# Optimization experiments

Hardware: AMD Instinct MI355X
Metric: run time of the kernel (lower is better)

## Reference

```python
import jax, jax.numpy as jnp
import numpy as np

N, E, IN_DIM, D, T, L, B, SLEN, C = 50000, 600000, 128, 128, 4, 2, 2048, 16, 16


def _deg_inv_sqrt(idx, n, dtype):
    deg = jax.ops.segment_sum(jnp.ones(idx.shape, dtype=dtype), idx, num_segments=n)
    return jnp.where(deg > 0, deg ** -0.5, 0.0).astype(dtype)


def gcn_conv(h, edge_index, W, b):
    # PyG GCNConv: add self loops, symmetric norm, x@W, scatter-add, +bias
    n = h.shape[0]
    loop = jnp.arange(n)
    row = jnp.concatenate([edge_index[0], loop])
    col = jnp.concatenate([edge_index[1], loop])
    dis = _deg_inv_sqrt(col, n, h.dtype)
    norm = dis[row] * dis[col]              # [E+N]
    xw = h @ W                               # [N, D]
    msgs = xw[row] * norm[:, None]           # [E+N, D] gather
    out = jax.ops.segment_sum(msgs, col, num_segments=n)
    return out + b


def re_conv(r, edge_index, node_type, W, wtype, b):
    # REConv(norm='both'): left-norm by src out-degree, x@W, type weight,
    # scatter-add to dst, right-norm by dst in-degree, +bias, relu
    n = r.shape[0]
    row, col = edge_index
    dl = _deg_inv_sqrt(row, n, r.dtype)
    x = (r * dl[:, None]) @ W                # [N, T]
    x = x * wtype[node_type][:, None]
    out = jax.ops.segment_sum(x[row], col, num_segments=n)
    dr = _deg_inv_sqrt(col, n, r.dtype)
    out = out * dr[:, None] + b
    return jax.nn.relu(out)


def setup_inputs() -> dict:
    key = jax.random.key(0)
    ks = jax.random.split(key, 10)
    x = jax.random.normal(ks[0], (N, IN_DIM), dtype=jnp.float32)
    label = jax.random.randint(ks[1], (N,), 0, C)
    seqs = jax.random.randint(ks[2], (B, SLEN), 0, N)
    edge_index = jax.random.randint(ks[3], (2, E), 0, N)
    node_type = jnp.sort(jax.random.randint(ks[4], (N,), 0, T))
    s_in = 1.0 / np.sqrt(IN_DIM)
    s_d = 1.0 / np.sqrt(D)
    fcW = jax.random.normal(ks[5], (T, IN_DIM, D), dtype=jnp.float32) * s_in
    fcB = jnp.zeros((T, D), dtype=jnp.float32)
    gcnW = jax.random.normal(ks[6], (L, D, D), dtype=jnp.float32) * s_d
    gcnB = jnp.zeros((L, D), dtype=jnp.float32)
    reW = jax.random.normal(ks[7], (L, T, T), dtype=jnp.float32) * 0.5
    re_wtype = jnp.ones((L, T), dtype=jnp.float32)
    reB = jnp.zeros((L, T), dtype=jnp.float32)
    predW = jax.random.normal(ks[8], (D, C), dtype=jnp.float32) * s_d
    predB = jnp.zeros((C,), dtype=jnp.float32)
    return {"x": x, "label": label, "seqs": seqs, "edge_index": edge_index,
            "node_type": node_type, "fcW": fcW, "fcB": fcB, "gcnW": gcnW,
            "gcnB": gcnB, "reW": reW, "re_wtype": re_wtype, "reB": reB,
            "predW": predW, "predB": predB}


def reference(x, label, seqs, edge_index, node_type, fcW, fcB, gcnW, gcnB,
              reW, re_wtype, reB, predW, predB):
    n = x.shape[0]
    # per-type input projection; node_type is sorted so this equals
    # torch.cat([fc[t](x[node_type==t]) for t])
    h_all = jnp.einsum('ni,tio->tno', x, fcW) + fcB[:, None, :]  # [T, N, D]
    gh = h_all[node_type, jnp.arange(n)]                          # [N, D]
    r = jnp.eye(fcW.shape[0], dtype=x.dtype)[node_type]           # [N, T]
    for l in range(gcnW.shape[0]):
        gh = jax.nn.relu(gcn_conv(gh, edge_index, gcnW[l], gcnB[l]))
        r = re_conv(r, edge_index, node_type, reW[l], re_wtype[l], reB[l])
    ego = seqs[:, 0]
    output = gh[ego] @ predW + predB                               # [B, C]
    return output, label[ego]
```

## Files before the change

kernel.cpp:

```cpp
#include <hip/hip_runtime.h>
#include <hip/hip_bf16.h>


typedef __attribute__((ext_vector_type(8))) short short8;
typedef __attribute__((ext_vector_type(4))) float f32x4;
typedef unsigned short u16;

__device__ __forceinline__ float bf2f(u16 u) {
  union { float f; unsigned int i; } v; v.i = (unsigned int)u << 16; return v.f;
}
__device__ __forceinline__ u16 f2bf(float f) {
  union { float f; unsigned int i; } v; v.f = f;
  return (u16)((v.i + 0x7FFF + ((v.i >> 16) & 1)) >> 16);
}

#define NPB 128
#define SWZ(row, byte) ((byte) ^ (((row) & 15) << 4))

__global__ void k_prep(const float* __restrict__ fcW, const float* __restrict__ gcnW,
                       u16* __restrict__ wt, int* __restrict__ ecnt,
                       int T, int wt_total, int n) {
  const int gt = blockIdx.x * 256 + threadIdx.x;
  const int GT = gridDim.x * 256;
  for (int i = gt; i < wt_total; i += GT) {
    int m = i >> 14, dk = i & 16383, d = dk >> 7, k = dk & 127;
    const float* src = (m < T) ? (fcW + ((size_t)m << 14)) : (gcnW + ((size_t)(m - T) << 14));
    wt[i] = f2bf(src[k * 128 + d]);
  }
  for (int i = gt; i < n; i += GT) ecnt[i] = 0;
}

__device__ __forceinline__ void stage_tile_bf16(char* smem, const u16* __restrict__ gsrc,
                                                int rows_valid, int t) {
  int row = t >> 1;
  int h = (t & 1) * 64;
  int byte0 = row * 256 + h * 2;
  if (row < rows_valid) {
    const u16* src = gsrc + (size_t)row * 128 + h;
#pragma unroll
    for (int j = 0; j < 8; ++j) {
      short8 v = *(const short8*)(src + j * 8);
      *(short8*)(smem + SWZ(row, byte0 + j * 16)) = v;
    }
  } else {
    short8 z = (short8){0, 0, 0, 0, 0, 0, 0, 0};
#pragma unroll
    for (int j = 0; j < 8; ++j)
      *(short8*)(smem + SWZ(row, byte0 + j * 16)) = z;
  }
}

__device__ __forceinline__ void mfma_core128(const char* xs, const char* wt, int t,
                                             f32x4 acc[8][2]) {
  const int lane = t & 63, w = t >> 6;
  const int lr = lane & 15, lk = lane >> 4;
  short8 bfrag[4][2];
#pragma unroll
  for (int ks = 0; ks < 4; ++ks) {
    int kb = ks * 64 + lk * 16;
#pragma unroll
    for (int ch = 0; ch < 2; ++ch) {
      int row = w * 32 + ch * 16 + lr;
      bfrag[ks][ch] = *(const short8*)(wt + SWZ(row, row * 256 + kb));
    }
  }
#pragma unroll
  for (int ks = 0; ks < 4; ++ks) {
    int kb = ks * 64 + lk * 16;
    short8 a[8];
#pragma unroll
    for (int rg = 0; rg < 8; ++rg) {
      int row = rg * 16 + lr;
      a[rg] = *(const short8*)(xs + SWZ(row, row * 256 + kb));
    }
#pragma unroll
    for (int rg = 0; rg < 8; ++rg)
#pragma unroll
      for (int ch = 0; ch < 2; ++ch)
        acc[rg][ch] = __builtin_amdgcn_mfma_f32_16x16x32_bf16(a[rg], bfrag[ks][ch],
                                                              acc[rg][ch], 0, 0, 0);
  }
}

__global__ __launch_bounds__(256) void k_fc(const float* __restrict__ x,
                                            const int* __restrict__ node_type,
                                            const u16* __restrict__ wt_fc,
                                            const float* __restrict__ fcB,
                                            u16* __restrict__ gh, int n_nodes,
                                            const int* __restrict__ col,
                                            int* __restrict__ ecnt, int e_edges) {
  __shared__ char smem[65536];
  char* smem_xs = smem;
  char* smem_wt = smem + 32768;
  const int t = threadIdx.x;
  const int nbase = blockIdx.x * NPB;
  const int nend = min(nbase + NPB, n_nodes);
  const int t0 = node_type[nbase];
  const int t1 = node_type[nend - 1];

  {
    int row = t >> 1;
    int h = (t & 1) * 64;
    int node = nbase + row;
    int byte0 = row * 256 + h * 2;
    if (node < n_nodes) {
      const float4* src = (const float4*)(x + (size_t)node * 128 + h);
#pragma unroll
      for (int j = 0; j < 8; ++j) {
        float4 a4 = src[j * 2], b4 = src[j * 2 + 1];
        u16 tmp[8] = {f2bf(a4.x), f2bf(a4.y), f2bf(a4.z), f2bf(a4.w),
                      f2bf(b4.x), f2bf(b4.y), f2bf(b4.z), f2bf(b4.w)};
        *(short8*)(smem_xs + SWZ(row, byte0 + j * 16)) = *(short8*)tmp;
      }
    } else {
      short8 z = (short8){0, 0, 0, 0, 0, 0, 0, 0};
#pragma unroll
      for (int j = 0; j < 8; ++j)
        *(short8*)(smem_xs + SWZ(row, byte0 + j * 16)) = z;
    }
  }

  const int lane = t & 63, w = t >> 6;
  const int lr = lane & 15, lk = lane >> 4;

  for (int tt = t0; tt <= t1; ++tt) {
    if (tt > t0) __syncthreads();
    stage_tile_bf16(smem_wt, wt_fc + ((size_t)tt << 14), 128, t);
    __syncthreads();

    f32x4 acc[8][2];
#pragma unroll
    for (int rg = 0; rg < 8; ++rg)
#pragma unroll
      for (int ch = 0; ch < 2; ++ch) acc[rg][ch] = (f32x4){0.f, 0.f, 0.f, 0.f};
    mfma_core128(smem_xs, smem_wt, t, acc);

    float bv0 = fcB[tt * 128 + w * 32 + lr];
    float bv1 = fcB[tt * 128 + w * 32 + 16 + lr];
#pragma unroll
    for (int rg = 0; rg < 8; ++rg) {
#pragma unroll
      for (int reg = 0; reg < 4; ++reg) {
        int node = nbase + rg * 16 + lk * 4 + reg;
        if (node < n_nodes && node_type[node] == tt) {
          gh[(size_t)node * 128 + w * 32 + lr]      = f2bf(acc[rg][0][reg] + bv0);
          gh[(size_t)node * 128 + w * 32 + 16 + lr] = f2bf(acc[rg][1][reg] + bv1);
        }
      }
    }
  }

  const int gt = blockIdx.x * 256 + t;
  const int GT = gridDim.x * 256;
  for (int i = gt; i < e_edges; i += GT) atomicAdd(&ecnt[col[i]], 1);
}

__global__ __launch_bounds__(256) void k_gemm_scale(const u16* __restrict__ ghin,
                                                    const u16* __restrict__ wtg,
                                                    const float* __restrict__ dis,
                                                    u16* __restrict__ xws, int n_nodes,
                                                    const int* __restrict__ row,
                                                    const int* __restrict__ col,
                                                    int* __restrict__ cursor,
                                                    int* __restrict__ edge_row,
                                                    int e_edges, int do_fill) {
  __shared__ char smem[65536];
  char* smem_xs = smem;
  char* smem_wt = smem + 32768;
  const int t = threadIdx.x;
  const int nbase = blockIdx.x * NPB;

  stage_tile_bf16(smem_xs, ghin + (size_t)nbase * 128, min(n_nodes - nbase, NPB), t);
  stage_tile_bf16(smem_wt, wtg, 128, t);
  __syncthreads();

  f32x4 acc[8][2];
#pragma unroll
  for (int rg = 0; rg < 8; ++rg)
#pragma unroll
    for (int ch = 0; ch < 2; ++ch) acc[rg][ch] = (f32x4){0.f, 0.f, 0.f, 0.f};
  mfma_core128(smem_xs, smem_wt, t, acc);

  const int lane = t & 63, w = t >> 6;
  const int lr = lane & 15, lk = lane >> 4;
#pragma unroll
  for (int rg = 0; rg < 8; ++rg) {
#pragma unroll
    for (int reg = 0; reg < 4; ++reg) {
      int node = nbase + rg * 16 + lk * 4 + reg;
      if (node < n_nodes) {
        float s = dis[node];
        xws[(size_t)node * 128 + w * 32 + lr]      = f2bf(acc[rg][0][reg] * s);
        xws[(size_t)node * 128 + w * 32 + 16 + lr] = f2bf(acc[rg][1][reg] * s);
      }
    }
  }

  if (do_fill) {
    const int gt = blockIdx.x * 256 + t;
    const int GT = gridDim.x * 256;
    for (int i = gt; i < e_edges; i += GT) {
      int c = col[i];
      int pos = atomicAdd(&cursor[c], 1);
      edge_row[pos] = row[i];
    }
  }
}

__global__ __launch_bounds__(256) void k_scan1(const int* __restrict__ ecnt,
                                               int* __restrict__ scanex,
                                               int* __restrict__ partials, int n) {
  __shared__ int s[256];
  const int t = threadIdx.x;
  const int i = blockIdx.x * 256 + t;
  int v = (i < n) ? ecnt[i] : 0;
  s[t] = v;
  __syncthreads();
  for (int off = 1; off < 256; off <<= 1) {
    int add = (t >= off) ? s[t - off] : 0;
    __syncthreads();
    s[t] += add;
    __syncthreads();
  }
  if (i < n) scanex[i] = s[t] - v;
  if (t == 255) partials[blockIdx.x] = s[t];
}

__global__ __launch_bounds__(256) void k_scan2(int* __restrict__ partials, int np) {
  __shared__ int s[256];
  const int t = threadIdx.x;
  int v = (t < np) ? partials[t] : 0;
  s[t] = v;
  __syncthreads();
  for (int off = 1; off < 256; off <<= 1) {
    int add = (t >= off) ? s[t - off] : 0;
    __syncthreads();
    s[t] += add;
    __syncthreads();
  }
  if (t < np) partials[t] = s[t] - v;
}

__global__ void k_scan3(const int* __restrict__ scanex, const int* __restrict__ partials,
                        const int* __restrict__ ecnt, int* __restrict__ col_ptr,
                        int* __restrict__ cursor, float* __restrict__ dis,
                        int n, int e_total) {
  int i = blockIdx.x * 256 + threadIdx.x;
  if (i < n) {
    int p = scanex[i] + partials[i >> 8];
    col_ptr[i] = p;
    cursor[i] = p;
    dis[i] = rsqrtf((float)(ecnt[i] + 1));
  }
  if (i == 0) col_ptr[n] = e_total;
}

__device__ __forceinline__ void gather_node(int node, const int* __restrict__ col_ptr,
                                            const int* __restrict__ edge_row,
                                            const u16* __restrict__ xws,
                                            const float* __restrict__ dis,
                                            const float* __restrict__ bias,
                                            u16* __restrict__ dst, int lane) {
  const int g = lane & 15;
  const int s = lane >> 4;
  float acc[8] = {0.f, 0.f, 0.f, 0.f, 0.f, 0.f, 0.f, 0.f};
  if (s == 0) {
    short8 v = *(const short8*)(xws + (size_t)node * 128 + g * 8);
#pragma unroll
    for (int j = 0; j < 8; ++j) acc[j] = bf2f((u16)v[j]);
  }
  const int e0 = col_ptr[node], e1 = col_ptr[node + 1];
  for (int e = e0 + s; e < e1; e += 4) {
    int r = edge_row[e];
    short8 v = *(const short8*)(xws + (size_t)r * 128 + g * 8);
#pragma unroll
    for (int j = 0; j < 8; ++j) acc[j] += bf2f((u16)v[j]);
  }
#pragma unroll
  for (int j = 0; j < 8; ++j) {
    acc[j] += __shfl_xor(acc[j], 16);
    acc[j] += __shfl_xor(acc[j], 32);
  }
  if (s == 0) {
    float ds = dis[node];
    u16 o[8];
#pragma unroll
    for (int j = 0; j < 8; ++j)
      o[j] = f2bf(fmaxf(acc[j] * ds + bias[g * 8 + j], 0.f));
    *(short8*)(dst + g * 8) = *(short8*)o;
  }
}

__global__ __launch_bounds__(256) void k_gather(const int* __restrict__ col_ptr,
                                                const int* __restrict__ edge_row,
                                                const u16* __restrict__ xws,
                                                const float* __restrict__ dis,
                                                const float* __restrict__ bias,
                                                u16* __restrict__ gh, int n_nodes) {
  const int t = threadIdx.x;
  const int node = blockIdx.x * 4 + (t >> 6);
  if (node >= n_nodes) return;
  gather_node(node, col_ptr, edge_row, xws, dis, bias,
              gh + (size_t)node * 128, t & 63);
}

__global__ __launch_bounds__(256) void k_egopred(const int* __restrict__ col_ptr,
                                                 const int* __restrict__ edge_row,
                                                 const u16* __restrict__ xws,
                                                 const float* __restrict__ dis,
                                                 const float* __restrict__ bias,
                                                 const int* __restrict__ seqs,
                                                 const int* __restrict__ label,
                                                 const float* __restrict__ predW,
                                                 const float* __restrict__ predB,
                                                 float* __restrict__ out,
                                                 float* __restrict__ out_label,
                                                 int b_total, int n_classes, int slen) {
  __shared__ u16 buf[4][128];
  const int t = threadIdx.x;
  const int w = t >> 6, lane = t & 63;
  const int b = blockIdx.x * 4 + w;
  int node = -1;
  if (b < b_total) {
    node = seqs[(size_t)b * slen];
    gather_node(node, col_ptr, edge_row, xws, dis, bias, &buf[w][0], lane);
  }
  __syncthreads();
  if (b < b_total) {
    const int c = lane & 15;
    const int q = lane >> 4;
    float s = 0.f;
#pragma unroll 8
    for (int k = q * 32; k < q * 32 + 32; ++k)
      s += bf2f(buf[w][k]) * predW[k * n_classes + c];
    s += __shfl_xor(s, 16);
    s += __shfl_xor(s, 32);
    if (q == 0) out[(size_t)b * n_classes + c] = s + predB[c];
    if (lane == 0) out_label[b] = (float)label[node];
  }
}

extern "C" void kernel_launch(void* const* d_in, const int* in_sizes, int n_in,
                              void* d_out, int out_size, void* d_ws, size_t ws_size,
                              hipStream_t stream) {
  const float* x     = (const float*)d_in[0];
  const int*   label = (const int*)d_in[1];
  const int*   seqs  = (const int*)d_in[2];
  const int*   edge  = (const int*)d_in[3];
  const int*   ntype = (const int*)d_in[4];
  const float* fcW   = (const float*)d_in[5];
  const float* fcB   = (const float*)d_in[6];
  const float* gcnW  = (const float*)d_in[7];
  const float* gcnB  = (const float*)d_in[8];
  const float* predW = (const float*)d_in[12];
  const float* predB = (const float*)d_in[13];

  const int n = in_sizes[0] / 128;
  const int e = in_sizes[3] / 2;
  const int T = in_sizes[5] / (128 * 128);
  const int L = in_sizes[8] / 128;
  const int C = in_sizes[13];
  const int slen = 16;
  const int b_total = in_sizes[2] / slen;

  const int* row = edge;
  const int* col = edge + e;

  char* ws = (char*)d_ws;
  const size_t node_bf = (size_t)n * 128 * sizeof(u16);
  u16*   gh      = (u16*)ws;                 ws += node_bf;
  u16*   xws     = (u16*)ws;                 ws += node_bf;
  u16*   wt      = (u16*)ws;                 ws += (size_t)(T + L) * 16384 * 2;
  float* dis     = (float*)ws;               ws += (size_t)n * 4;
  int*   ecnt    = (int*)ws;                 ws += (size_t)n * 4;
  int*   scanex  = (int*)ws;                 ws += (size_t)n * 4;
  int*   col_ptr = (int*)ws;                 ws += (size_t)(n + 16) * 4;
  int*   cursor  = (int*)ws;                 ws += (size_t)n * 4;
  int*   partial = (int*)ws;                 ws += 1024 * 4;
  int*   edge_row= (int*)ws;                 ws += (size_t)e * 4;

  float* out_logits = (float*)d_out;
  float* out_label  = out_logits + (size_t)b_total * C;

  const int nb = (n + NPB - 1) / NPB;
  const int nscan = (n + 255) / 256;
  const int wt_total = (T + L) * 16384;

  hipLaunchKernelGGL(k_prep, dim3(384), dim3(256), 0, stream,
                     fcW, gcnW, wt, ecnt, T, wt_total, n);
  hipLaunchKernelGGL(k_fc, dim3(nb), dim3(256), 0, stream,
                     x, ntype, wt, fcB, gh, n, col, ecnt, e);
  hipLaunchKernelGGL(k_scan1, dim3(nscan), dim3(256), 0, stream, ecnt, scanex, partial, n);
  hipLaunchKernelGGL(k_scan2, dim3(1), dim3(256), 0, stream, partial, nscan);
  hipLaunchKernelGGL(k_scan3, dim3(nscan), dim3(256), 0, stream, scanex, partial, ecnt,
                     col_ptr, cursor, dis, n, e);

  for (int l = 0; l < L; ++l) {
    hipLaunchKernelGGL(k_gemm_scale, dim3(nb), dim3(256), 0, stream,
                       gh, wt + (size_t)(T + l) * 16384, dis, xws, n,
                       row, col, cursor, edge_row, e, (l == 0) ? 1 : 0);
    if (l < L - 1) {
      hipLaunchKernelGGL(k_gather, dim3((n + 3) / 4), dim3(256), 0, stream,
                         col_ptr, edge_row, xws, dis, gcnB + (size_t)l * 128, gh, n);
    } else {
      hipLaunchKernelGGL(k_egopred, dim3((b_total + 3) / 4), dim3(256), 0, stream,
                         col_ptr, edge_row, xws, dis, gcnB + (size_t)l * 128,
                         seqs, label, predW, predB, out_logits, out_label,
                         b_total, C, slen);
    }
  }
}
```

Baseline: 248.6 us.

## Load GEMM weights directly from global and fuse scan phases via last-block pattern

```diff
diff --git a/kernel.cpp b/kernel.cpp
--- a/kernel.cpp
+++ b/kernel.cpp
@@ -19,7 +19,7 @@
 
 __global__ void k_prep(const float* __restrict__ fcW, const float* __restrict__ gcnW,
                        u16* __restrict__ wt, int* __restrict__ ecnt,
-                       int T, int wt_total, int n) {
+                       int* __restrict__ cnt, int T, int wt_total, int n) {
   const int gt = blockIdx.x * 256 + threadIdx.x;
   const int GT = gridDim.x * 256;
   for (int i = gt; i < wt_total; i += GT) {
@@ -28,6 +28,7 @@
     wt[i] = f2bf(src[k * 128 + d]);
   }
   for (int i = gt; i < n; i += GT) ecnt[i] = 0;
+  if (gt == 0) *cnt = 0;
 }
 
 __device__ __forceinline__ void stage_tile_bf16(char* smem, const u16* __restrict__ gsrc,
@@ -50,20 +51,18 @@
   }
 }
 
-__device__ __forceinline__ void mfma_core128(const char* xs, const char* wt, int t,
-                                             f32x4 acc[8][2]) {
+__device__ __forceinline__ void mfma_core128_g(const char* xs, const u16* __restrict__ wtg,
+                                               int t, f32x4 acc[8][2]) {
   const int lane = t & 63, w = t >> 6;
   const int lr = lane & 15, lk = lane >> 4;
   short8 bfrag[4][2];
 #pragma unroll
-  for (int ks = 0; ks < 4; ++ks) {
-    int kb = ks * 64 + lk * 16;
+  for (int ks = 0; ks < 4; ++ks)
 #pragma unroll
     for (int ch = 0; ch < 2; ++ch) {
       int row = w * 32 + ch * 16 + lr;
-      bfrag[ks][ch] = *(const short8*)(wt + SWZ(row, row * 256 + kb));
-    }
-  }
+      bfrag[ks][ch] = *(const short8*)(wtg + (size_t)row * 128 + ks * 32 + lk * 8);
+    }
 #pragma unroll
   for (int ks = 0; ks < 4; ++ks) {
     int kb = ks * 64 + lk * 16;
@@ -89,9 +88,7 @@
                                             u16* __restrict__ gh, int n_nodes,
                                             const int* __restrict__ col,
                                             int* __restrict__ ecnt, int e_edges) {
-  __shared__ char smem[65536];
-  char* smem_xs = smem;
-  char* smem_wt = smem + 32768;
+  __shared__ char smem_xs[32768];
   const int t = threadIdx.x;
   const int nbase = blockIdx.x * NPB;
   const int nend = min(nbase + NPB, n_nodes);
@@ -119,21 +116,18 @@
         *(short8*)(smem_xs + SWZ(row, byte0 + j * 16)) = z;
     }
   }
+  __syncthreads();
 
   const int lane = t & 63, w = t >> 6;
   const int lr = lane & 15, lk = lane >> 4;
 
   for (int tt = t0; tt <= t1; ++tt) {
-    if (tt > t0) __syncthreads();
-    stage_tile_bf16(smem_wt, wt_fc + ((size_t)tt << 14), 128, t);
-    __syncthreads();
-
     f32x4 acc[8][2];
 #pragma unroll
     for (int rg = 0; rg < 8; ++rg)
 #pragma unroll
       for (int ch = 0; ch < 2; ++ch) acc[rg][ch] = (f32x4){0.f, 0.f, 0.f, 0.f};
-    mfma_core128(smem_xs, smem_wt, t, acc);
+    mfma_core128_g(smem_xs, wt_fc + ((size_t)tt << 14), t, acc);
 
     float bv0 = fcB[tt * 128 + w * 32 + lr];
     float bv1 = fcB[tt * 128 + w * 32 + 16 + lr];
@@ -164,14 +158,11 @@
                                                     int* __restrict__ cursor,
                                                     int* __restrict__ edge_row,
                                                     int e_edges, int do_fill) {
-  __shared__ char smem[65536];
-  char* smem_xs = smem;
-  char* smem_wt = smem + 32768;
+  __shared__ char smem_xs[32768];
   const int t = threadIdx.x;
   const int nbase = blockIdx.x * NPB;
 
   stage_tile_bf16(smem_xs, ghin + (size_t)nbase * 128, min(n_nodes - nbase, NPB), t);
-  stage_tile_bf16(smem_wt, wtg, 128, t);
   __syncthreads();
 
   f32x4 acc[8][2];
@@ -179,7 +170,7 @@
   for (int rg = 0; rg < 8; ++rg)
 #pragma unroll
     for (int ch = 0; ch < 2; ++ch) acc[rg][ch] = (f32x4){0.f, 0.f, 0.f, 0.f};
-  mfma_core128(smem_xs, smem_wt, t, acc);
+  mfma_core128_g(smem_xs, wtg, t, acc);
 
   const int lane = t & 63, w = t >> 6;
   const int lr = lane & 15, lk = lane >> 4;
@@ -209,8 +200,11 @@
 
 __global__ __launch_bounds__(256) void k_scan1(const int* __restrict__ ecnt,
                                                int* __restrict__ scanex,
-                                               int* __restrict__ partials, int n) {
+                                               int* __restrict__ partials,
+                                               float* __restrict__ dis,
+                                               int* __restrict__ cnt, int n) {
   __shared__ int s[256];
+  __shared__ int lastflag;
   const int t = threadIdx.x;
   const int i = blockIdx.x * 256 + t;
   int v = (i < n) ? ecnt[i] : 0;
@@ -222,35 +216,38 @@
     s[t] += add;
     __syncthreads();
   }
-  if (i < n) scanex[i] = s[t] - v;
+  if (i < n) {
+    scanex[i] = s[t] - v;
+    dis[i] = rsqrtf((float)(v + 1));
+  }
   if (t == 255) partials[blockIdx.x] = s[t];
-}
-
-__global__ __launch_bounds__(256) void k_scan2(int* __restrict__ partials, int np) {
-  __shared__ int s[256];
-  const int t = threadIdx.x;
-  int v = (t < np) ? partials[t] : 0;
-  s[t] = v;
+  __threadfence();
+  if (t == 0) lastflag = (atomicAdd(cnt, 1) == gridDim.x - 1) ? 1 : 0;
   __syncthreads();
-  for (int off = 1; off < 256; off <<= 1) {
-    int add = (t >= off) ? s[t - off] : 0;
+  if (lastflag) {
+    __threadfence();
+    int np = gridDim.x;
+    int pv = (t < np) ? partials[t] : 0;
+    s[t] = pv;
     __syncthreads();
-    s[t] += add;
-    __syncthreads();
-  }
-  if (t < np) partials[t] = s[t] - v;
+    for (int off = 1; off < 256; off <<= 1) {
+      int add = (t >= off) ? s[t - off] : 0;
+      __syncthreads();
+      s[t] += add;
+      __syncthreads();
+    }
+    if (t < np) partials[t] = s[t] - pv;
+  }
 }
 
 __global__ void k_scan3(const int* __restrict__ scanex, const int* __restrict__ partials,
-                        const int* __restrict__ ecnt, int* __restrict__ col_ptr,
-                        int* __restrict__ cursor, float* __restrict__ dis,
+                        int* __restrict__ col_ptr, int* __restrict__ cursor,
                         int n, int e_total) {
   int i = blockIdx.x * 256 + threadIdx.x;
   if (i < n) {
     int p = scanex[i] + partials[i >> 8];
     col_ptr[i] = p;
     cursor[i] = p;
-    dis[i] = rsqrtf((float)(ecnt[i] + 1));
   }
   if (i == 0) col_ptr[n] = e_total;
 }
@@ -377,6 +374,7 @@
   int*   col_ptr = (int*)ws;                 ws += (size_t)(n + 16) * 4;
   int*   cursor  = (int*)ws;                 ws += (size_t)n * 4;
   int*   partial = (int*)ws;                 ws += 1024 * 4;
+  int*   cnt     = (int*)ws;                 ws += 64;
   int*   edge_row= (int*)ws;                 ws += (size_t)e * 4;
 
   float* out_logits = (float*)d_out;
@@ -387,13 +385,13 @@
   const int wt_total = (T + L) * 16384;
 
   hipLaunchKernelGGL(k_prep, dim3(384), dim3(256), 0, stream,
-                     fcW, gcnW, wt, ecnt, T, wt_total, n);
+                     fcW, gcnW, wt, ecnt, cnt, T, wt_total, n);
   hipLaunchKernelGGL(k_fc, dim3(nb), dim3(256), 0, stream,
                      x, ntype, wt, fcB, gh, n, col, ecnt, e);
-  hipLaunchKernelGGL(k_scan1, dim3(nscan), dim3(256), 0, stream, ecnt, scanex, partial, n);
-  hipLaunchKernelGGL(k_scan2, dim3(1), dim3(256), 0, stream, partial, nscan);
-  hipLaunchKernelGGL(k_scan3, dim3(nscan), dim3(256), 0, stream, scanex, partial, ecnt,
-                     col_ptr, cursor, dis, n, e);
+  hipLaunchKernelGGL(k_scan1, dim3(nscan), dim3(256), 0, stream,
+                     ecnt, scanex, partial, dis, cnt, n);
+  hipLaunchKernelGGL(k_scan3, dim3(nscan), dim3(256), 0, stream,
+                     scanex, partial, col_ptr, cursor, n, e);
 
   for (int l = 0; l < L; ++l) {
     hipLaunchKernelGGL(k_gemm_scale, dim3(nb), dim3(256), 0, stream,
```

Result: slower. 256.5 us (+3.2%).
